# Optimization experiments

Hardware: AMD Instinct MI355X
Metric: run time of the kernel (lower is better)

## Reference

```python
import jax, jax.numpy as jnp
import numpy as np

B, N, D, E, H = 8, 128, 64, 3, 256
L = E + 1  # edge label 0 = 'no edge' (dropped by edge_types[:, 1:])
DEC_OUT = 64


def setup_inputs() -> dict:
    key = jax.random.key(0)
    ks = jax.random.split(key, 8)
    node_states = jax.random.normal(ks[0], (B, 1, N, D), dtype=jnp.float32)
    # one-hot edge-type labels [B, N, N, L]
    type_ids = jax.random.randint(ks[1], (B, N, N), 0, L)
    edges = jax.nn.one_hot(type_ids, L, dtype=jnp.float32)
    def lin(k, fan_in, shape):
        return jax.random.normal(k, shape, dtype=jnp.float32) / jnp.sqrt(jnp.float32(fan_in))
    return {
        "node_states": node_states,
        "edges": edges,
        # per-edge-type encoder MLP (2 layers, relu after each)
        "We1": lin(ks[2], 2 * D, (E, 2 * D, H)),
        "be1": jnp.zeros((E, H), dtype=jnp.float32),
        "We2": lin(ks[3], H, (E, H, H)),
        "be2": jnp.zeros((E, H), dtype=jnp.float32),
        # node decoder MLP (2 layers, relu after each)
        "Wd1": lin(ks[4], D + H, (D + H, H)),
        "bd1": jnp.zeros((H,), dtype=jnp.float32),
        "Wd2": lin(ks[5], H, (H, DEC_OUT)),
        "bd2": jnp.zeros((DEC_OUT,), dtype=jnp.float32),
    }


def reference(node_states, edges, We1, be1, We2, be2, Wd1, bd1, Wd2, bd2):
    b, _, n, d = node_states.shape
    ns = node_states[:, 0]  # [B, N, D]
    # NodePropagator: for fully-connected edges, the one-hot matmuls are a
    # gather: edge e = (i, j) gets [ns[i], ns[j]] (flat index i*N + j).
    msg_src = jnp.broadcast_to(ns[:, :, None, :], (b, n, n, d))  # source i
    msg_tgt = jnp.broadcast_to(ns[:, None, :, :], (b, n, n, d))  # target j
    node_msgs = jnp.concatenate([msg_src, msg_tgt], -1).reshape(b, n * n, 2 * d)
    # EdgeEncoder: one 2-layer relu MLP per edge type -> [B, E, N^2, H]
    h = jax.nn.relu(jnp.einsum("bmd,edh->bemh", node_msgs, We1) + be1[None, :, None, :])
    h = jax.nn.relu(jnp.einsum("bemh,ehk->bemk", h, We2) + be2[None, :, None, :])
    # mask by edge-type indicator; type 0 (no edge) is dropped
    edge_types = jnp.transpose(edges.reshape(b, n * n, L), (0, 2, 1))  # [B, L, N^2]
    edge_msgs = h * edge_types[:, 1:, :, None]  # [B, E, N^2, H]
    # EdgeAggregator: edge_targets^T matmul = scatter-sum over sources i per
    # target j, then sum over edge types (dim 1, keepdim).
    aggr = edge_msgs.reshape(b, E, n, n, H).sum(axis=2)  # [B, E, N, H]
    aggr = aggr.sum(axis=1, keepdims=True)  # [B, 1, N, H]
    # node decoder
    dec_in = jnp.concatenate([node_states, aggr], -1)  # [B, 1, N, D+H]
    out = jax.nn.relu(dec_in @ Wd1 + bd1)
    out = jax.nn.relu(out @ Wd2 + bd2)
    return out  # [B, 1, N, DEC_OUT]
```

## Files before the change

### kernel.cpp

```cpp
#include <hip/hip_runtime.h>

#define NB 8
#define NN 128
#define ND 64
#define NE 3
#define NH 256
#define NOUT 64

typedef short bf16x8_t __attribute__((ext_vector_type(8)));
typedef float f32x4_t __attribute__((ext_vector_type(4)));
typedef unsigned short ushort_t;

static __device__ __forceinline__ unsigned short f2bf(float f) {
    unsigned u = __float_as_uint(f);
    u += 0x7FFFu + ((u >> 16) & 1u);
    return (unsigned short)(u >> 16);
}
static __device__ __forceinline__ unsigned pk2bf(float a, float b) {
    return (unsigned)f2bf(a) | ((unsigned)f2bf(b) << 16);
}

static __device__ __forceinline__ bf16x8_t a_genf(float4 p0, float4 p1, float4 q0, float4 q1) {
    union { uint4 u; bf16x8_t v; } r;
    r.u.x = pk2bf(fmaxf(p0.x + q0.x, 0.f), fmaxf(p0.y + q0.y, 0.f));
    r.u.y = pk2bf(fmaxf(p0.z + q0.z, 0.f), fmaxf(p0.w + q0.w, 0.f));
    r.u.z = pk2bf(fmaxf(p1.x + q1.x, 0.f), fmaxf(p1.y + q1.y, 0.f));
    r.u.w = pk2bf(fmaxf(p1.z + q1.z, 0.f), fmaxf(p1.w + q1.w, 0.f));
    return r.v;
}

#define IT 16
__global__ __launch_bounds__(256) void prep_kernel(
    const float* __restrict__ We2, const float* __restrict__ ns,
    const float* __restrict__ We1, const float* __restrict__ be1,
    const float* __restrict__ edges,
    ushort_t* __restrict__ We2p,
    float* __restrict__ P, float* __restrict__ Q,
    ushort_t* __restrict__ list_ws, int4* __restrict__ cnts_ws)
{
    const int t = threadIdx.x;
    const int blk = blockIdx.x;

    if (blk < 48) {
        __shared__ float slab[256][16];
        const int e = blk >> 4, nfg = blk & 15;
        const int n0 = nfg * 16;
#pragma unroll
        for (int it = 0; it < 16; it++) {
            const int k = (t >> 4) + it * 16;
            slab[k][t & 15] = We2[((size_t)e * NH + k) * NH + n0 + (t & 15)];
        }
        __syncthreads();
        ushort_t* dst = We2p + ((size_t)e * 16 + nfg) * 4096;
#pragma unroll
        for (int it = 0; it < 16; it++) {
            const int idx = it * 256 + t;
            const int kk = idx >> 9;
            const int ln = (idx >> 3) & 63;
            const int jj = idx & 7;
            const int k = kk * 32 + (ln >> 4) * 8 + jj;
            dst[idx] = f2bf(slab[k][ln & 15]);
        }
        return;
    }
    if (blk < 240) {
        __shared__ float ns_lds[IT][ND];
        const int blk2 = blk - 48;
        const int itile = blk2 & 7;
        const int e = (blk2 >> 3) % NE;
        const int b = blk2 / 24;
        const int i0 = itile * IT;
        for (int x = t; x < IT * ND; x += 256)
            ns_lds[x / ND][x % ND] = ns[(size_t)(b * NN + i0 + x / ND) * ND + (x % ND)];
        __syncthreads();
        const int h = t;
        float accP[IT], accQ[IT];
        const float bias = be1[e * NH + h];
#pragma unroll
        for (int m = 0; m < IT; m++) { accP[m] = 0.f; accQ[m] = bias; }
        const float* W1 = We1 + (size_t)e * 2 * ND * NH + h;
        for (int d = 0; d < ND; d++) {
            const float w1 = W1[(size_t)d * NH];
            const float w2 = W1[(size_t)(ND + d) * NH];
#pragma unroll
            for (int m = 0; m < IT; m++) {
                accP[m] = fmaf(ns_lds[m][d], w1, accP[m]);
                accQ[m] = fmaf(ns_lds[m][d], w2, accQ[m]);
            }
        }
#pragma unroll
        for (int m = 0; m < IT; m++) {
            const size_t idx = ((size_t)((b * NE + e) * NN) + i0 + m) * NH + h;
            P[idx] = accP[m];
            Q[idx] = accQ[m];
        }
        return;
    }
    {
        __shared__ unsigned long long wm[2][NE];
        const int pb = blk - 240;
        const int b = pb >> 7, j = pb & 127;
        const int lane = t & 63, wave = t >> 6;
        int ecls = -1;
        if (t < 128) {
            const float4 ev = *(const float4*)(edges + ((size_t)(b * NN + t) * NN + j) * 4);
            ecls = ev.y > 0.5f ? 0 : (ev.z > 0.5f ? 1 : (ev.w > 0.5f ? 2 : -1));
#pragma unroll
            for (int ee = 0; ee < NE; ee++) {
                unsigned long long m = __ballot(ecls == ee);
                if (lane == 0) wm[wave][ee] = m;
            }
        }
        __syncthreads();
        const int c0 = __popcll(wm[0][0]) + __popcll(wm[1][0]);
        const int c1 = __popcll(wm[0][1]) + __popcll(wm[1][1]);
        const int c2 = __popcll(wm[0][2]) + __popcll(wm[1][2]);
        if (t < 128 && ecls >= 0) {
            const unsigned long long lower = (1ull << lane) - 1ull;
            int pos = __popcll(wm[wave][ecls] & lower);
            if (wave == 1) pos += __popcll(wm[0][ecls]);
            pos += (ecls > 0 ? c0 : 0) + (ecls > 1 ? c1 : 0);
            list_ws[(size_t)pb * NN + pos] = (ushort_t)t;
        }
        if (t == 0) { int4 cc; cc.x = c0; cc.y = c1; cc.z = c2; cc.w = 0; cnts_ws[pb] = cc; }
    }
}

__global__ __launch_bounds__(512) void gemm_kernel(
    const float* __restrict__ Pf,
    const float* __restrict__ Qf,
    const ushort_t* __restrict__ We2p,
    const float* __restrict__ be2,
    const ushort_t* __restrict__ list_ws,
    const int4* __restrict__ cnts_ws,
    float* __restrict__ aggr3)
{
    const int blk = blockIdx.x;
    const int jg = blk & 15;
    const int e  = (blk >> 4) % 3;
    const int b  = blk / 48;
    const int tid = threadIdx.x;
    const int lane = tid & 63;
    const int wave = tid >> 6;

    __shared__ __align__(16) ushort_t Bl[16 * 8 * 512];

    {
        const ushort_t* Bsrc = We2p + (size_t)e * 65536;
#pragma unroll
        for (int it = 0; it < 16; it++) {
            const int o = it * 4096 + tid * 8;
            *(uint4*)&Bl[o] = *(const uint4*)&Bsrc[o];
        }
    }

    const int j = jg * 8 + wave;
    const int4 cc = cnts_ws[b * NN + j];
    const int ce = e == 0 ? cc.x : (e == 1 ? cc.y : cc.z);
    const int start = (e > 0 ? cc.x : 0) + (e > 1 ? cc.y : 0);
    const ushort_t* Lj = list_ws + (size_t)(b * NN + j) * NN + start;
    const float* Qj = Qf + (size_t)((b * NE + e) * NN + j) * NH;
    const float* Pb = Pf + (size_t)(b * NE + e) * NN * NH;

    float bb[16];
#pragma unroll
    for (int nf = 0; nf < 16; nf++)
        bb[nf] = be2[e * NH + nf * 16 + (lane & 15)];

    __syncthreads();

    float rsum[16];
#pragma unroll
    for (int nf = 0; nf < 16; nf++) rsum[nf] = 0.f;

    if (ce > 0) {
        const int F = (ce + 15) >> 4;
        for (int f = 0; f < F; f++) {
            int p = f * 16 + (lane & 15);
            p = p < ce ? p : ce - 1;
            const float* P0 = Pb + (size_t)Lj[p] * NH;

            f32x4_t acc[16];
            const f32x4_t z4 = {0.f, 0.f, 0.f, 0.f};
#pragma unroll
            for (int nf = 0; nf < 16; nf++) acc[nf] = z4;

#pragma unroll 2
            for (int kk = 0; kk < 8; kk++) {
                const int ko = kk * 32 + (lane >> 4) * 8;
                const float4 q0 = *(const float4*)(Qj + ko);
                const float4 q1 = *(const float4*)(Qj + ko + 4);
                const float4 p0 = *(const float4*)(P0 + ko);
                const float4 p1 = *(const float4*)(P0 + ko + 4);
                const bf16x8_t af = a_genf(p0, p1, q0, q1);
#pragma unroll
                for (int nf = 0; nf < 16; nf++) {
                    const bf16x8_t bfr = *(const bf16x8_t*)(&Bl[(nf * 8 + kk) * 512 + lane * 8]);
                    acc[nf] = __builtin_amdgcn_mfma_f32_16x16x32_bf16(af, bfr, acc[nf], 0, 0, 0);
                }
            }
#pragma unroll
            for (int nf = 0; nf < 16; nf++) {
                float s = 0.f;
#pragma unroll
                for (int r = 0; r < 4; r++) {
                    const int pos = f * 16 + ((lane >> 4) << 2) + r;
                    if (pos < ce) s += fmaxf(acc[nf][r] + bb[nf], 0.f);
                }
                s += __shfl_xor(s, 16, 64);
                s += __shfl_xor(s, 32, 64);
                if (lane < 16) rsum[nf] += s;
            }
        }
    }
    if (lane < 16) {
        float* dst = aggr3 + (size_t)((b * NE + e) * NN + j) * NH + lane;
#pragma unroll
        for (int nf = 0; nf < 16; nf++) dst[nf * 16] = rsum[nf];
    }
}

__global__ __launch_bounds__(256) void dec_kernel(
    const float* __restrict__ ns,
    const float* __restrict__ aggr3,
    const float* __restrict__ Wd1, const float* __restrict__ bd1,
    const float* __restrict__ Wd2, const float* __restrict__ bd2,
    float* __restrict__ out)
{
    const int b = blockIdx.x >> 4;
    const int jg = blockIdx.x & 15;
    const int tid = threadIdx.x;
    __shared__ __align__(16) float xs[8][320];
    __shared__ __align__(16) float o1s[8][NH];

    for (int x = tid; x < 8 * 320; x += 256) {
        const int jj = x / 320, k = x % 320;
        const int j = jg * 8 + jj;
        float v;
        if (k < ND) v = ns[(size_t)(b * NN + j) * ND + k];
        else {
            const int c = k - ND;
            v = aggr3[(size_t)((b * NE + 0) * NN + j) * NH + c]
              + aggr3[(size_t)((b * NE + 1) * NN + j) * NH + c]
              + aggr3[(size_t)((b * NE + 2) * NN + j) * NH + c];
        }
        xs[jj][k] = v;
    }
    __syncthreads();
    {
        const int n = tid;
        float acc[8];
        const float b1 = bd1[n];
#pragma unroll
        for (int jj = 0; jj < 8; jj++) acc[jj] = b1;
        for (int k4 = 0; k4 < 80; k4++) {
            const float w0 = Wd1[(size_t)(k4 * 4 + 0) * NH + n];
            const float w1 = Wd1[(size_t)(k4 * 4 + 1) * NH + n];
            const float w2 = Wd1[(size_t)(k4 * 4 + 2) * NH + n];
            const float w3 = Wd1[(size_t)(k4 * 4 + 3) * NH + n];
#pragma unroll
            for (int jj = 0; jj < 8; jj++) {
                const float4 xv = *(const float4*)(&xs[jj][k4 * 4]);
                acc[jj] = fmaf(xv.x, w0, fmaf(xv.y, w1, fmaf(xv.z, w2, fmaf(xv.w, w3, acc[jj]))));
            }
        }
#pragma unroll
        for (int jj = 0; jj < 8; jj++) o1s[jj][n] = fmaxf(acc[jj], 0.f);
    }
    __syncthreads();
    {
        const int jj = tid >> 5, cp = tid & 31;
        const int n0 = cp * 2;
        float a0 = bd2[n0], a1 = bd2[n0 + 1];
        for (int h4 = 0; h4 < 64; h4++) {
            const float4 ov = *(const float4*)(&o1s[jj][h4 * 4]);
            a0 = fmaf(ov.x, Wd2[(size_t)(h4 * 4 + 0) * NOUT + n0], a0);
            a1 = fmaf(ov.x, Wd2[(size_t)(h4 * 4 + 0) * NOUT + n0 + 1], a1);
            a0 = fmaf(ov.y, Wd2[(size_t)(h4 * 4 + 1) * NOUT + n0], a0);
            a1 = fmaf(ov.y, Wd2[(size_t)(h4 * 4 + 1) * NOUT + n0 + 1], a1);
            a0 = fmaf(ov.z, Wd2[(size_t)(h4 * 4 + 2) * NOUT + n0], a0);
            a1 = fmaf(ov.z, Wd2[(size_t)(h4 * 4 + 2) * NOUT + n0 + 1], a1);
            a0 = fmaf(ov.w, Wd2[(size_t)(h4 * 4 + 3) * NOUT + n0], a0);
            a1 = fmaf(ov.w, Wd2[(size_t)(h4 * 4 + 3) * NOUT + n0 + 1], a1);
        }
        const int j = jg * 8 + jj;
        out[(size_t)(b * NN + j) * NOUT + n0] = fmaxf(a0, 0.f);
        out[(size_t)(b * NN + j) * NOUT + n0 + 1] = fmaxf(a1, 0.f);
    }
}

extern "C" void kernel_launch(void* const* d_in, const int* in_sizes, int n_in,
                              void* d_out, int out_size, void* d_ws, size_t ws_size,
                              hipStream_t stream)
{
    const float* ns    = (const float*)d_in[0];
    const float* edges = (const float*)d_in[1];
    const float* We1   = (const float*)d_in[2];
    const float* be1   = (const float*)d_in[3];
    const float* We2   = (const float*)d_in[4];
    const float* be2   = (const float*)d_in[5];
    const float* Wd1   = (const float*)d_in[6];
    const float* bd1   = (const float*)d_in[7];
    const float* Wd2   = (const float*)d_in[8];
    const float* bd2   = (const float*)d_in[9];
    float* outp = (float*)d_out;

    float* Pf = (float*)d_ws;
    float* Qf = Pf + (size_t)NB * NE * NN * NH;
    ushort_t* We2p = (ushort_t*)(Qf + (size_t)NB * NE * NN * NH);
    ushort_t* list_ws = We2p + (size_t)NE * NH * NH;
    int4* cnts_ws = (int4*)(list_ws + (size_t)NB * NN * NN);
    float* aggr3 = (float*)(cnts_ws + NB * NN);

    hipLaunchKernelGGL(prep_kernel, dim3(1264), dim3(256), 0, stream,
                       We2, ns, We1, be1, edges, We2p, Pf, Qf, list_ws, cnts_ws);
    hipLaunchKernelGGL(gemm_kernel, dim3(384), dim3(512), 0, stream,
                       Pf, Qf, We2p, be2, list_ws, cnts_ws, aggr3);
    hipLaunchKernelGGL(dec_kernel, dim3(NB * 16), dim3(256), 0, stream,
                       ns, aggr3, Wd1, bd1, Wd2, bd2, outp);
}
```

Measured before the change: 83.45 us.

## Split gemm output columns across blocks and process two targets per wave

The edge-MLP second-layer kernel now splits the 256 hidden outputs into two halves across blocks, so each block stages only half of the We2 tile in LDS (64KB instead of 128KB). Each wave handles two target nodes, which reuses every LDS B fragment for two MFMAs and doubles the independent MFMA chains. Blocks shrink to 256 threads and the grid doubles to 768, aiming at more resident blocks per CU. In exchange, the A-side P/Q gathers and relu conversion are repeated for both column halves, and a wave runs for as many chunks as the larger of its two targets' edge counts.

```diff
diff --git a/kernel.cpp b/kernel.cpp
--- a/kernel.cpp
+++ b/kernel.cpp
@@ -126,7 +126,7 @@
     }
 }
 
-__global__ __launch_bounds__(512) void gemm_kernel(
+__global__ __launch_bounds__(256) void gemm_kernel(
     const float* __restrict__ Pf,
     const float* __restrict__ Qf,
     const ushort_t* __restrict__ We2p,
@@ -136,87 +136,103 @@
     float* __restrict__ aggr3)
 {
     const int blk = blockIdx.x;
-    const int jg = blk & 15;
-    const int e  = (blk >> 4) % 3;
-    const int b  = blk / 48;
+    const int nh = blk & 1;
+    const int jg = (blk >> 1) & 15;
+    const int e  = (blk >> 5) % 3;
+    const int b  = blk / 96;
     const int tid = threadIdx.x;
     const int lane = tid & 63;
     const int wave = tid >> 6;
 
-    __shared__ __align__(16) ushort_t Bl[16 * 8 * 512];
+    __shared__ __align__(16) ushort_t Bl[8 * 8 * 512];
 
     {
-        const ushort_t* Bsrc = We2p + (size_t)e * 65536;
+        const ushort_t* Bsrc = We2p + ((size_t)e * 16 + nh * 8) * 4096;
 #pragma unroll
         for (int it = 0; it < 16; it++) {
-            const int o = it * 4096 + tid * 8;
+            const int o = it * 2048 + tid * 8;
             *(uint4*)&Bl[o] = *(const uint4*)&Bsrc[o];
         }
     }
 
-    const int j = jg * 8 + wave;
-    const int4 cc = cnts_ws[b * NN + j];
-    const int ce = e == 0 ? cc.x : (e == 1 ? cc.y : cc.z);
-    const int start = (e > 0 ? cc.x : 0) + (e > 1 ? cc.y : 0);
-    const ushort_t* Lj = list_ws + (size_t)(b * NN + j) * NN + start;
-    const float* Qj = Qf + (size_t)((b * NE + e) * NN + j) * NH;
+    const int j0 = jg * 8 + wave * 2;
+    const int j1 = j0 + 1;
+    const int4 cc0 = cnts_ws[b * NN + j0];
+    const int4 cc1 = cnts_ws[b * NN + j1];
+    const int ce0 = e == 0 ? cc0.x : (e == 1 ? cc0.y : cc0.z);
+    const int ce1 = e == 0 ? cc1.x : (e == 1 ? cc1.y : cc1.z);
+    const int st0 = (e > 0 ? cc0.x : 0) + (e > 1 ? cc0.y : 0);
+    const int st1 = (e > 0 ? cc1.x : 0) + (e > 1 ? cc1.y : 0);
+    const ushort_t* L0 = list_ws + (size_t)(b * NN + j0) * NN + st0;
+    const ushort_t* L1 = list_ws + (size_t)(b * NN + j1) * NN + st1;
+    const float* Q0 = Qf + (size_t)((b * NE + e) * NN + j0) * NH;
+    const float* Q1 = Qf + (size_t)((b * NE + e) * NN + j1) * NH;
     const float* Pb = Pf + (size_t)(b * NE + e) * NN * NH;
 
-    float bb[16];
-#pragma unroll
-    for (int nf = 0; nf < 16; nf++)
-        bb[nf] = be2[e * NH + nf * 16 + (lane & 15)];
+    float bb[8];
+#pragma unroll
+    for (int nf = 0; nf < 8; nf++)
+        bb[nf] = be2[e * NH + nh * 128 + nf * 16 + (lane & 15)];
 
     __syncthreads();
 
-    float rsum[16];
-#pragma unroll
-    for (int nf = 0; nf < 16; nf++) rsum[nf] = 0.f;
-
-    if (ce > 0) {
-        const int F = (ce + 15) >> 4;
+    float rs0[8], rs1[8];
+#pragma unroll
+    for (int nf = 0; nf < 8; nf++) { rs0[nf] = 0.f; rs1[nf] = 0.f; }
+
+    const int cemax = ce0 > ce1 ? ce0 : ce1;
+    if (cemax > 0) {
+        const int F = (cemax + 15) >> 4;
         for (int f = 0; f < F; f++) {
-            int p = f * 16 + (lane & 15);
-            p = p < ce ? p : ce - 1;
-            const float* P0 = Pb + (size_t)Lj[p] * NH;
-
-            f32x4_t acc[16];
+            const int lm = f * 16 + (lane & 15);
+            const int q0i = lm < ce0 ? lm : (ce0 > 0 ? ce0 - 1 : 0);
+            const int q1i = lm < ce1 ? lm : (ce1 > 0 ? ce1 - 1 : 0);
+            const int row0 = ce0 > 0 ? L0[q0i] : 0;
+            const int row1 = ce1 > 0 ? L1[q1i] : 0;
+            const float* P0 = Pb + (size_t)row0 * NH;
+            const float* P1 = Pb + (size_t)row1 * NH;
+
+            f32x4_t a0c[8], a1c[8];
             const f32x4_t z4 = {0.f, 0.f, 0.f, 0.f};
 #pragma unroll
-            for (int nf = 0; nf < 16; nf++) acc[nf] = z4;
+            for (int nf = 0; nf < 8; nf++) { a0c[nf] = z4; a1c[nf] = z4; }
 
 #pragma unroll 2
             for (int kk = 0; kk < 8; kk++) {
                 const int ko = kk * 32 + (lane >> 4) * 8;
-                const float4 q0 = *(const float4*)(Qj + ko);
-                const float4 q1 = *(const float4*)(Qj + ko + 4);
-                const float4 p0 = *(const float4*)(P0 + ko);
-                const float4 p1 = *(const float4*)(P0 + ko + 4);
-                const bf16x8_t af = a_genf(p0, p1, q0, q1);
-#pragma unroll
-                for (int nf = 0; nf < 16; nf++) {
+                const bf16x8_t af0 = a_genf(*(const float4*)(P0 + ko), *(const float4*)(P0 + ko + 4),
+                                            *(const float4*)(Q0 + ko), *(const float4*)(Q0 + ko + 4));
+                const bf16x8_t af1 = a_genf(*(const float4*)(P1 + ko), *(const float4*)(P1 + ko + 4),
+                                            *(const float4*)(Q1 + ko), *(const float4*)(Q1 + ko + 4));
+#pragma unroll
+                for (int nf = 0; nf < 8; nf++) {
                     const bf16x8_t bfr = *(const bf16x8_t*)(&Bl[(nf * 8 + kk) * 512 + lane * 8]);
-                    acc[nf] = __builtin_amdgcn_mfma_f32_16x16x32_bf16(af, bfr, acc[nf], 0, 0, 0);
+                    a0c[nf] = __builtin_amdgcn_mfma_f32_16x16x32_bf16(af0, bfr, a0c[nf], 0, 0, 0);
+                    a1c[nf] = __builtin_amdgcn_mfma_f32_16x16x32_bf16(af1, bfr, a1c[nf], 0, 0, 0);
                 }
             }
 #pragma unroll
-            for (int nf = 0; nf < 16; nf++) {
-                float s = 0.f;
+            for (int nf = 0; nf < 8; nf++) {
+                float s0 = 0.f, s1 = 0.f;
 #pragma unroll
                 for (int r = 0; r < 4; r++) {
                     const int pos = f * 16 + ((lane >> 4) << 2) + r;
-                    if (pos < ce) s += fmaxf(acc[nf][r] + bb[nf], 0.f);
+                    if (pos < ce0) s0 += fmaxf(a0c[nf][r] + bb[nf], 0.f);
+                    if (pos < ce1) s1 += fmaxf(a1c[nf][r] + bb[nf], 0.f);
                 }
-                s += __shfl_xor(s, 16, 64);
-                s += __shfl_xor(s, 32, 64);
-                if (lane < 16) rsum[nf] += s;
+                s0 += __shfl_xor(s0, 16, 64);
+                s0 += __shfl_xor(s0, 32, 64);
+                s1 += __shfl_xor(s1, 16, 64);
+                s1 += __shfl_xor(s1, 32, 64);
+                if (lane < 16) { rs0[nf] += s0; rs1[nf] += s1; }
             }
         }
     }
     if (lane < 16) {
-        float* dst = aggr3 + (size_t)((b * NE + e) * NN + j) * NH + lane;
-#pragma unroll
-        for (int nf = 0; nf < 16; nf++) dst[nf * 16] = rsum[nf];
+        float* d0 = aggr3 + (size_t)((b * NE + e) * NN + j0) * NH + nh * 128 + lane;
+        float* d1 = aggr3 + (size_t)((b * NE + e) * NN + j1) * NH + nh * 128 + lane;
+#pragma unroll
+        for (int nf = 0; nf < 8; nf++) { d0[nf * 16] = rs0[nf]; d1[nf * 16] = rs1[nf]; }
     }
 }
 
@@ -314,7 +330,7 @@
 
     hipLaunchKernelGGL(prep_kernel, dim3(1264), dim3(256), 0, stream,
                        We2, ns, We1, be1, edges, We2p, Pf, Qf, list_ws, cnts_ws);
-    hipLaunchKernelGGL(gemm_kernel, dim3(384), dim3(512), 0, stream,
+    hipLaunchKernelGGL(gemm_kernel, dim3(768), dim3(256), 0, stream,
                        Pf, Qf, We2p, be2, list_ws, cnts_ws, aggr3);
     hipLaunchKernelGGL(dec_kernel, dim3(NB * 16), dim3(256), 0, stream,
                        ns, aggr3, Wd1, bd1, Wd2, bd2, outp);
```

Result: slower. 111.6 us (+33.8%).
